# Kernel tuning notes

Measured on AMD Instinct MI355X. Metric: run time of the kernel, lower is better.

Reference implementation:

```python
import jax, jax.numpy as jnp
import numpy as np

EPS = 1e-06


def setup_inputs() -> dict:
    key = jax.random.key(0)
    B, T, M = 64, 8000, 80
    x = jax.random.uniform(key, (B, T, M), dtype=jnp.float32)
    # learned params are stored in log-space, per-mel, matching the torch module
    log_s = jnp.full((M,), np.log(0.0001), dtype=jnp.float32)
    log_alpha = jnp.full((M,), np.log(0.98), dtype=jnp.float32)
    log_delta = jnp.full((M,), np.log(2.0), dtype=jnp.float32)
    log_r = jnp.full((M,), np.log(0.2), dtype=jnp.float32)
    return {"x": x, "log_s": log_s, "log_alpha": log_alpha,
            "log_delta": log_delta, "log_r": log_r}


def reference(x, log_s, log_alpha, log_delta, log_r):
    # PCEN: leaky-integrator EMA over time + power-law compression.
    s = jnp.exp(log_s)          # [M]
    alpha = jnp.exp(log_alpha)  # [M]
    delta = jnp.exp(log_delta)  # [M]
    r = jnp.exp(log_r)          # [M]
    delta_r = delta ** r

    B, T, M = x.shape
    xt = jnp.swapaxes(x, 0, 1)  # [T, B, M] so scan streams over time

    def step(m_prev, frame):  # m_prev, frame: [B, M]
        m_cur = (1.0 - s) * m_prev + s * frame
        out = (frame / (m_cur + EPS) ** alpha + delta) ** r - delta_r
        return m_cur, out

    m0 = jnp.zeros((B, M), dtype=x.dtype)
    _, out_t = jax.lax.scan(step, m0, xt)  # [T, B, M]
    return jnp.swapaxes(out_t, 0, 1)       # [B, T, M]
```

## Files before the change

kernel.cpp:

```cpp
#include <hip/hip_runtime.h>
#include <math.h>

#define PCEN_EPS 1e-6f


__global__ void pcen_chunk_scan_v4(const float4* __restrict__ x,
                                   const float* __restrict__ log_s,
                                   float4* __restrict__ contrib,
                                   int B, int T, int M4, int C, int L) {
    int tid = blockIdx.x * blockDim.x + threadIdx.x;
    int total = B * C * M4;
    if (tid >= total) return;
    int g = tid % M4;
    int c = (tid / M4) % C;
    int b = tid / (M4 * C);

    float sx = expf(log_s[4 * g + 0]);
    float sy = expf(log_s[4 * g + 1]);
    float sz = expf(log_s[4 * g + 2]);
    float sw = expf(log_s[4 * g + 3]);
    float ox = 1.0f - sx, oy = 1.0f - sy, oz = 1.0f - sz, ow = 1.0f - sw;

    int start = c * L;
    int len = T - start;
    if (len > L) len = L;
    if (len < 0) len = 0;

    int base = (b * T + start) * M4 + g;
    float mx = 0.0f, my = 0.0f, mz = 0.0f, mw = 0.0f;
#pragma unroll 8
    for (int i = 0; i < len; ++i) {
        float4 xv = x[base];
        mx = fmaf(ox, mx, sx * xv.x);
        my = fmaf(oy, my, sy * xv.y);
        mz = fmaf(oz, mz, sz * xv.z);
        mw = fmaf(ow, mw, sw * xv.w);
        base += M4;
    }
    float4 o;
    o.x = mx; o.y = my; o.z = mz; o.w = mw;
    contrib[tid] = o;
}

__global__ void pcen_chunk_prefix_v4(const float4* __restrict__ contrib,
                                     const float* __restrict__ log_s,
                                     float4* __restrict__ m_start,
                                     int B, int T, int M4, int C, int L) {
    int tid = blockIdx.x * blockDim.x + threadIdx.x;
    if (tid >= B * M4) return;
    int g = tid % M4;
    int b = tid / M4;

    float sx = expf(log_s[4 * g + 0]);
    float sy = expf(log_s[4 * g + 1]);
    float sz = expf(log_s[4 * g + 2]);
    float sw = expf(log_s[4 * g + 3]);
    float ox = 1.0f - sx, oy = 1.0f - sy, oz = 1.0f - sz, ow = 1.0f - sw;
    float dxf = powf(ox, (float)L);
    float dyf = powf(oy, (float)L);
    float dzf = powf(oz, (float)L);
    float dwf = powf(ow, (float)L);

    int base = b * C * M4 + g;
    float mx = 0.0f, my = 0.0f, mz = 0.0f, mw = 0.0f;
#pragma unroll 4
    for (int c = 0; c < C; ++c) {
        float4 o;
        o.x = mx; o.y = my; o.z = mz; o.w = mw;
        m_start[base + c * M4] = o;

        int start = c * L;
        int len = T - start;
        if (len > L) len = L;
        if (len < 0) len = 0;

        float fx = dxf, fy = dyf, fz = dzf, fw = dwf;
        if (len != L) {
            fx = powf(ox, (float)len);
            fy = powf(oy, (float)len);
            fz = powf(oz, (float)len);
            fw = powf(ow, (float)len);
        }
        float4 cv = contrib[base + c * M4];
        mx = fmaf(fx, mx, cv.x);
        my = fmaf(fy, my, cv.y);
        mz = fmaf(fz, mz, cv.z);
        mw = fmaf(fw, mw, cv.w);
    }
}

__global__ void pcen_output_v4(const float4* __restrict__ x,
                               const float* __restrict__ log_s,
                               const float* __restrict__ log_alpha,
                               const float* __restrict__ log_delta,
                               const float* __restrict__ log_r,
                               const float4* __restrict__ m_start,
                               float4* __restrict__ out,
                               int B, int T, int M4, int C, int L) {
    int tid = blockIdx.x * blockDim.x + threadIdx.x;
    int total = B * C * M4;
    if (tid >= total) return;
    int g = tid % M4;
    int c = (tid / M4) % C;
    int b = tid / (M4 * C);

    float sx = expf(log_s[4 * g + 0]);
    float sy = expf(log_s[4 * g + 1]);
    float sz = expf(log_s[4 * g + 2]);
    float sw = expf(log_s[4 * g + 3]);
    float ox = 1.0f - sx, oy = 1.0f - sy, oz = 1.0f - sz, ow = 1.0f - sw;

    float ax = expf(log_alpha[4 * g + 0]);
    float ay = expf(log_alpha[4 * g + 1]);
    float az = expf(log_alpha[4 * g + 2]);
    float aw = expf(log_alpha[4 * g + 3]);

    float dx = expf(log_delta[4 * g + 0]);
    float dy = expf(log_delta[4 * g + 1]);
    float dz = expf(log_delta[4 * g + 2]);
    float dw = expf(log_delta[4 * g + 3]);

    float rx = expf(log_r[4 * g + 0]);
    float ry = expf(log_r[4 * g + 1]);
    float rz = expf(log_r[4 * g + 2]);
    float rw = expf(log_r[4 * g + 3]);

    float drx = powf(dx, rx);
    float dry = powf(dy, ry);
    float drz = powf(dz, rz);
    float drw = powf(dw, rw);

    int start = c * L;
    int len = T - start;
    if (len > L) len = L;
    if (len < 0) len = 0;

    float4 m0 = m_start[tid];
    float mx = m0.x, my = m0.y, mz = m0.z, mw = m0.w;

    int base = (b * T + start) * M4 + g;
#pragma unroll 4
    for (int i = 0; i < len; ++i) {
        float4 xv = x[base];
        mx = fmaf(ox, mx, sx * xv.x);
        my = fmaf(oy, my, sy * xv.y);
        mz = fmaf(oz, mz, sz * xv.z);
        mw = fmaf(ow, mw, sw * xv.w);

        float4 o;
        float px = __expf(-ax * __logf(mx + PCEN_EPS));
        float py = __expf(-ay * __logf(my + PCEN_EPS));
        float pz = __expf(-az * __logf(mz + PCEN_EPS));
        float pw = __expf(-aw * __logf(mw + PCEN_EPS));
        float yx = fmaf(xv.x, px, dx);
        float yy = fmaf(xv.y, py, dy);
        float yz = fmaf(xv.z, pz, dz);
        float yw = fmaf(xv.w, pw, dw);
        o.x = __expf(rx * __logf(yx)) - drx;
        o.y = __expf(ry * __logf(yy)) - dry;
        o.z = __expf(rz * __logf(yz)) - drz;
        o.w = __expf(rw * __logf(yw)) - drw;

        out[base] = o;
        base += M4;
    }
}


__global__ void pcen_chunk_scan(const float* __restrict__ x,
                                const float* __restrict__ log_s,
                                float* __restrict__ contrib,
                                int B, int T, int M, int C, int L) {
    int tid = blockIdx.x * blockDim.x + threadIdx.x;
    int total = B * C * M;
    if (tid >= total) return;
    int mi = tid % M;
    int c  = (tid / M) % C;
    int b  = tid / (M * C);

    float s   = expf(log_s[mi]);
    float oms = 1.0f - s;

    int start = c * L;
    int len = T - start;
    if (len > L) len = L;
    if (len < 0) len = 0;

    int base = (b * T + start) * M + mi;
    float m = 0.0f;
#pragma unroll 4
    for (int i = 0; i < len; ++i) {
        m = fmaf(oms, m, s * x[base]);
        base += M;
    }
    contrib[tid] = m;
}

__global__ void pcen_chunk_prefix(const float* __restrict__ contrib,
                                  const float* __restrict__ log_s,
                                  float* __restrict__ m_start,
                                  int B, int T, int M, int C, int L) {
    int tid = blockIdx.x * blockDim.x + threadIdx.x;
    if (tid >= B * M) return;
    int mi = tid % M;
    int b  = tid / M;

    float s   = expf(log_s[mi]);
    float oms = 1.0f - s;
    float dL_full = powf(oms, (float)L);

    int base = b * C * M + mi;
    float m = 0.0f;
    for (int c = 0; c < C; ++c) {
        m_start[base + c * M] = m;
        int start = c * L;
        int len = T - start;
        if (len > L) len = L;
        if (len < 0) len = 0;
        float dL = (len == L) ? dL_full : powf(oms, (float)len);
        m = fmaf(dL, m, contrib[base + c * M]);
    }
}

__global__ void pcen_output(const float* __restrict__ x,
                            const float* __restrict__ log_s,
                            const float* __restrict__ log_alpha,
                            const float* __restrict__ log_delta,
                            const float* __restrict__ log_r,
                            const float* __restrict__ m_start,
                            float* __restrict__ out,
                            int B, int T, int M, int C, int L) {
    int tid = blockIdx.x * blockDim.x + threadIdx.x;
    int total = B * C * M;
    if (tid >= total) return;
    int mi = tid % M;
    int c  = (tid / M) % C;
    int b  = tid / (M * C);

    float s     = expf(log_s[mi]);
    float alpha = expf(log_alpha[mi]);
    float delta = expf(log_delta[mi]);
    float r     = expf(log_r[mi]);
    float delta_r = powf(delta, r);
    float oms   = 1.0f - s;

    int start = c * L;
    int len = T - start;
    if (len > L) len = L;
    if (len < 0) len = 0;

    float m = m_start[tid];
    int base = (b * T + start) * M + mi;
#pragma unroll 4
    for (int i = 0; i < len; ++i) {
        float xv = x[base];
        m = fmaf(oms, m, s * xv);
        float p = __expf(-alpha * __logf(m + PCEN_EPS));
        float y = fmaf(xv, p, delta);
        out[base] = __expf(r * __logf(y)) - delta_r;
        base += M;
    }
}

extern "C" void kernel_launch(void* const* d_in, const int* in_sizes, int n_in,
                              void* d_out, int out_size, void* d_ws, size_t ws_size,
                              hipStream_t stream) {
    const float* x         = (const float*)d_in[0];
    const float* log_s     = (const float*)d_in[1];
    const float* log_alpha = (const float*)d_in[2];
    const float* log_delta = (const float*)d_in[3];
    const float* log_r     = (const float*)d_in[4];
    float* out = (float*)d_out;

    const int M = in_sizes[1];
    const int B = 64;
    const int T = in_sizes[0] / (B * M);

    int C = 200;
    while (C > 1 && (size_t)(2ll * B * C * M * 4) > ws_size) C--;
    const int L = (T + C - 1) / C;

    float* contrib = (float*)d_ws;
    float* mstart  = contrib + (size_t)B * C * M;

    const int threads = 256;

    if ((M & 3) == 0) {
        const int M4 = M / 4;
        int total1 = B * C * M4;
        int total2 = B * M4;
        pcen_chunk_scan_v4<<<(total1 + threads - 1) / threads, threads, 0, stream>>>(
            (const float4*)x, log_s, (float4*)contrib, B, T, M4, C, L);
        pcen_chunk_prefix_v4<<<(total2 + threads - 1) / threads, threads, 0, stream>>>(
            (const float4*)contrib, log_s, (float4*)mstart, B, T, M4, C, L);
        pcen_output_v4<<<(total1 + threads - 1) / threads, threads, 0, stream>>>(
            (const float4*)x, log_s, log_alpha, log_delta, log_r,
            (const float4*)mstart, (float4*)out, B, T, M4, C, L);
    } else {
        int total1 = B * C * M;
        int total2 = B * M;
        pcen_chunk_scan<<<(total1 + threads - 1) / threads, threads, 0, stream>>>(
            x, log_s, contrib, B, T, M, C, L);
        pcen_chunk_prefix<<<(total2 + threads - 1) / threads, threads, 0, stream>>>(
            contrib, log_s, mstart, B, T, M, C, L);
        pcen_output<<<(total1 + threads - 1) / threads, threads, 0, stream>>>(
            x, log_s, log_alpha, log_delta, log_r, mstart, out, B, T, M, C, L);
    }
}
```

Before: 393.6 us.

## Fuse chunked PCEN scan into single-pass decoupled look-back kernel

Replaces the three-kernel chunk scan, prefix and output pipeline with one kernel. Blocks take a dynamic ticket and publish per-chunk aggregates and inclusive prefixes with status flags, and later chunks resolve their starting state by look-back over earlier chunks. This removes a kernel launch and the global round-trip of the contrib and m_start buffers. It adds a reset kernel, spin-waiting on atomics, and serial look-back latency. The fallback path's chunk count also changes.

```diff
diff --git a/kernel.cpp b/kernel.cpp
--- a/kernel.cpp
+++ b/kernel.cpp
@@ -3,145 +3,118 @@
 
 #define PCEN_EPS 1e-6f
 
-
-__global__ void pcen_chunk_scan_v4(const float4* __restrict__ x,
-                                   const float* __restrict__ log_s,
-                                   float4* __restrict__ contrib,
-                                   int B, int T, int M4, int C, int L) {
-    int tid = blockIdx.x * blockDim.x + threadIdx.x;
-    int total = B * C * M4;
-    if (tid >= total) return;
-    int g = tid % M4;
-    int c = (tid / M4) % C;
-    int b = tid / (M4 * C);
-
-    float sx = expf(log_s[4 * g + 0]);
-    float sy = expf(log_s[4 * g + 1]);
-    float sz = expf(log_s[4 * g + 2]);
-    float sw = expf(log_s[4 * g + 3]);
-    float ox = 1.0f - sx, oy = 1.0f - sy, oz = 1.0f - sz, ow = 1.0f - sw;
-
-    int start = c * L;
+__global__ void pcen_reset(int* __restrict__ p, int n) {
+    int i = blockIdx.x * blockDim.x + threadIdx.x;
+    int stride = gridDim.x * blockDim.x;
+    for (; i < n; i += stride) p[i] = 0;
+}
+
+__global__ __launch_bounds__(256) void pcen_fused_v4(
+    const float4* __restrict__ x,
+    const float* __restrict__ log_s,
+    const float* __restrict__ log_alpha,
+    const float* __restrict__ log_delta,
+    const float* __restrict__ log_r,
+    float4* __restrict__ aggbuf,
+    float4* __restrict__ inclbuf,
+    int* __restrict__ status,
+    int* __restrict__ ticket,
+    float4* __restrict__ out,
+    int B, int T, int G, int C, int L)
+{
+    __shared__ int svb;
+    if (threadIdx.x == 0) svb = atomicAdd(ticket, 1);
+    __syncthreads();
+    const int vtid = svb * (int)blockDim.x + (int)threadIdx.x;
+    const int BG = B * G;
+    const int c = vtid / BG;
+    if (c >= C) return;
+    const int rem = vtid - c * BG;
+    const int b = rem / G;
+    const int g = rem - b * G;
+
+    const float4 lsv = ((const float4*)log_s)[g];
+    const float sx = expf(lsv.x), sy = expf(lsv.y), sz = expf(lsv.z), sw = expf(lsv.w);
+    const float ox = 1.0f - sx, oy = 1.0f - sy, oz = 1.0f - sz, ow = 1.0f - sw;
+
+    const int start = c * L;
     int len = T - start;
     if (len > L) len = L;
     if (len < 0) len = 0;
 
-    int base = (b * T + start) * M4 + g;
-    float mx = 0.0f, my = 0.0f, mz = 0.0f, mw = 0.0f;
+    const int base0 = (b * T + start) * G + g;
+    float mx = 0.f, my = 0.f, mz = 0.f, mw = 0.f;
+    {
+        int p = base0;
 #pragma unroll 8
-    for (int i = 0; i < len; ++i) {
-        float4 xv = x[base];
-        mx = fmaf(ox, mx, sx * xv.x);
-        my = fmaf(oy, my, sy * xv.y);
-        mz = fmaf(oz, mz, sz * xv.z);
-        mw = fmaf(ow, mw, sw * xv.w);
-        base += M4;
-    }
-    float4 o;
-    o.x = mx; o.y = my; o.z = mz; o.w = mw;
-    contrib[tid] = o;
-}
-
-__global__ void pcen_chunk_prefix_v4(const float4* __restrict__ contrib,
-                                     const float* __restrict__ log_s,
-                                     float4* __restrict__ m_start,
-                                     int B, int T, int M4, int C, int L) {
-    int tid = blockIdx.x * blockDim.x + threadIdx.x;
-    if (tid >= B * M4) return;
-    int g = tid % M4;
-    int b = tid / M4;
-
-    float sx = expf(log_s[4 * g + 0]);
-    float sy = expf(log_s[4 * g + 1]);
-    float sz = expf(log_s[4 * g + 2]);
-    float sw = expf(log_s[4 * g + 3]);
-    float ox = 1.0f - sx, oy = 1.0f - sy, oz = 1.0f - sz, ow = 1.0f - sw;
-    float dxf = powf(ox, (float)L);
-    float dyf = powf(oy, (float)L);
-    float dzf = powf(oz, (float)L);
-    float dwf = powf(ow, (float)L);
-
-    int base = b * C * M4 + g;
-    float mx = 0.0f, my = 0.0f, mz = 0.0f, mw = 0.0f;
-#pragma unroll 4
-    for (int c = 0; c < C; ++c) {
-        float4 o;
-        o.x = mx; o.y = my; o.z = mz; o.w = mw;
-        m_start[base + c * M4] = o;
-
-        int start = c * L;
-        int len = T - start;
-        if (len > L) len = L;
-        if (len < 0) len = 0;
-
-        float fx = dxf, fy = dyf, fz = dzf, fw = dwf;
-        if (len != L) {
-            fx = powf(ox, (float)len);
-            fy = powf(oy, (float)len);
-            fz = powf(oz, (float)len);
-            fw = powf(ow, (float)len);
-        }
-        float4 cv = contrib[base + c * M4];
-        mx = fmaf(fx, mx, cv.x);
-        my = fmaf(fy, my, cv.y);
-        mz = fmaf(fz, mz, cv.z);
-        mw = fmaf(fw, mw, cv.w);
-    }
-}
-
-__global__ void pcen_output_v4(const float4* __restrict__ x,
-                               const float* __restrict__ log_s,
-                               const float* __restrict__ log_alpha,
-                               const float* __restrict__ log_delta,
-                               const float* __restrict__ log_r,
-                               const float4* __restrict__ m_start,
-                               float4* __restrict__ out,
-                               int B, int T, int M4, int C, int L) {
-    int tid = blockIdx.x * blockDim.x + threadIdx.x;
-    int total = B * C * M4;
-    if (tid >= total) return;
-    int g = tid % M4;
-    int c = (tid / M4) % C;
-    int b = tid / (M4 * C);
-
-    float sx = expf(log_s[4 * g + 0]);
-    float sy = expf(log_s[4 * g + 1]);
-    float sz = expf(log_s[4 * g + 2]);
-    float sw = expf(log_s[4 * g + 3]);
-    float ox = 1.0f - sx, oy = 1.0f - sy, oz = 1.0f - sz, ow = 1.0f - sw;
-
-    float ax = expf(log_alpha[4 * g + 0]);
-    float ay = expf(log_alpha[4 * g + 1]);
-    float az = expf(log_alpha[4 * g + 2]);
-    float aw = expf(log_alpha[4 * g + 3]);
-
-    float dx = expf(log_delta[4 * g + 0]);
-    float dy = expf(log_delta[4 * g + 1]);
-    float dz = expf(log_delta[4 * g + 2]);
-    float dw = expf(log_delta[4 * g + 3]);
-
-    float rx = expf(log_r[4 * g + 0]);
-    float ry = expf(log_r[4 * g + 1]);
-    float rz = expf(log_r[4 * g + 2]);
-    float rw = expf(log_r[4 * g + 3]);
-
-    float drx = powf(dx, rx);
-    float dry = powf(dy, ry);
-    float drz = powf(dz, rz);
-    float drw = powf(dw, rw);
-
-    int start = c * L;
-    int len = T - start;
-    if (len > L) len = L;
-    if (len < 0) len = 0;
-
-    float4 m0 = m_start[tid];
-    float mx = m0.x, my = m0.y, mz = m0.z, mw = m0.w;
-
-    int base = (b * T + start) * M4 + g;
+        for (int i = 0; i < len; ++i) {
+            float4 xv = x[p];
+            mx = fmaf(ox, mx, sx * xv.x);
+            my = fmaf(oy, my, sy * xv.y);
+            mz = fmaf(oz, mz, sz * xv.z);
+            mw = fmaf(ow, mw, sw * xv.w);
+            p += G;
+        }
+    }
+    const int sidx = vtid;
+    float4 a; a.x = mx; a.y = my; a.z = mz; a.w = mw;
+    aggbuf[sidx] = a;
+    if (c == 0) {
+        inclbuf[sidx] = a;
+        __hip_atomic_store(&status[sidx], 2, __ATOMIC_RELEASE, __HIP_MEMORY_SCOPE_AGENT);
+    } else {
+        __hip_atomic_store(&status[sidx], 1, __ATOMIC_RELEASE, __HIP_MEMORY_SCOPE_AGENT);
+    }
+
+    const float dLx = powf(ox, (float)L);
+    const float dLy = powf(oy, (float)L);
+    const float dLz = powf(oz, (float)L);
+    const float dLw = powf(ow, (float)L);
+    float msx = 0.f, msy = 0.f, msz = 0.f, msw = 0.f;
+    if (c > 0) {
+        float wx = 1.f, wy = 1.f, wz = 1.f, ww = 1.f;
+        int j = c - 1;
+        while (j >= 0) {
+            const int jidx = j * BG + rem;
+            int st;
+            while ((st = __hip_atomic_load(&status[jidx], __ATOMIC_ACQUIRE,
+                                           __HIP_MEMORY_SCOPE_AGENT)) == 0) {
+                __builtin_amdgcn_s_sleep(1);
+            }
+            const float4 v = (st == 2) ? inclbuf[jidx] : aggbuf[jidx];
+            msx = fmaf(wx, v.x, msx);
+            msy = fmaf(wy, v.y, msy);
+            msz = fmaf(wz, v.z, msz);
+            msw = fmaf(ww, v.w, msw);
+            if (st == 2) break;
+            wx *= dLx; wy *= dLy; wz *= dLz; ww *= dLw;
+            --j;
+        }
+        if (c < C - 1) {
+            float4 ic;
+            ic.x = fmaf(dLx, msx, a.x);
+            ic.y = fmaf(dLy, msy, a.y);
+            ic.z = fmaf(dLz, msz, a.z);
+            ic.w = fmaf(dLw, msw, a.w);
+            inclbuf[sidx] = ic;
+            __hip_atomic_store(&status[sidx], 2, __ATOMIC_RELEASE, __HIP_MEMORY_SCOPE_AGENT);
+        }
+    }
+
+    const float4 lav = ((const float4*)log_alpha)[g];
+    const float4 ldv = ((const float4*)log_delta)[g];
+    const float4 lrv = ((const float4*)log_r)[g];
+    const float ax = expf(lav.x), ay = expf(lav.y), az = expf(lav.z), aw = expf(lav.w);
+    const float dx = expf(ldv.x), dy = expf(ldv.y), dz = expf(ldv.z), dw = expf(ldv.w);
+    const float rx = expf(lrv.x), ry = expf(lrv.y), rz = expf(lrv.z), rw = expf(lrv.w);
+    const float drx = powf(dx, rx), dry = powf(dy, ry);
+    const float drz = powf(dz, rz), drw = powf(dw, rw);
+
+    mx = msx; my = msy; mz = msz; mw = msw;
+    int p = base0;
 #pragma unroll 4
     for (int i = 0; i < len; ++i) {
-        float4 xv = x[base];
+        float4 xv = x[p];
         mx = fmaf(ox, mx, sx * xv.x);
         my = fmaf(oy, my, sy * xv.y);
         mz = fmaf(oz, mz, sz * xv.z);
@@ -161,11 +134,10 @@
         o.z = __expf(rz * __logf(yz)) - drz;
         o.w = __expf(rw * __logf(yw)) - drw;
 
-        out[base] = o;
-        base += M4;
-    }
-}
-
+        out[p] = o;
+        p += G;
+    }
+}
 
 __global__ void pcen_chunk_scan(const float* __restrict__ x,
                                 const float* __restrict__ log_s,
@@ -276,27 +248,43 @@
     const int B = 64;
     const int T = in_sizes[0] / (B * M);
 
-    int C = 200;
-    while (C > 1 && (size_t)(2ll * B * C * M * 4) > ws_size) C--;
-    const int L = (T + C - 1) / C;
-
-    float* contrib = (float*)d_ws;
-    float* mstart  = contrib + (size_t)B * C * M;
-
-    const int threads = 256;
-
     if ((M & 3) == 0) {
-        const int M4 = M / 4;
-        int total1 = B * C * M4;
-        int total2 = B * M4;
-        pcen_chunk_scan_v4<<<(total1 + threads - 1) / threads, threads, 0, stream>>>(
-            (const float4*)x, log_s, (float4*)contrib, B, T, M4, C, L);
-        pcen_chunk_prefix_v4<<<(total2 + threads - 1) / threads, threads, 0, stream>>>(
-            (const float4*)contrib, log_s, (float4*)mstart, B, T, M4, C, L);
-        pcen_output_v4<<<(total1 + threads - 1) / threads, threads, 0, stream>>>(
+        const int G = M / 4;
+        int C = 200;
+        while (C > 1) {
+            long long N = (long long)B * C * G;
+            if ((size_t)(N * 36ll + 256) <= ws_size) break;
+            --C;
+        }
+        int L = (T + C - 1) / C;
+        C = (T + L - 1) / L;
+        const long long N = (long long)B * C * G;
+
+        float4* aggbuf  = (float4*)d_ws;
+        float4* inclbuf = aggbuf + N;
+        int*    status  = (int*)(inclbuf + N);
+        int*    ticket  = status + N;
+
+        const int nz = (int)N + 16;
+        int zgrid = (nz + 256 * 4 - 1) / (256 * 4);
+        if (zgrid < 1) zgrid = 1;
+        pcen_reset<<<zgrid, 256, 0, stream>>>(status, nz);
+
+        const int total = (int)N;
+        const int blocks = (total + 255) / 256;
+        pcen_fused_v4<<<blocks, 256, 0, stream>>>(
             (const float4*)x, log_s, log_alpha, log_delta, log_r,
-            (const float4*)mstart, (float4*)out, B, T, M4, C, L);
+            aggbuf, inclbuf, status, ticket, (float4*)out,
+            B, T, G, C, L);
     } else {
+        int C = 50;
+        while (C > 1 && (size_t)(2ll * B * C * M * 4) > ws_size) C--;
+        const int L = (T + C - 1) / C;
+
+        float* contrib = (float*)d_ws;
+        float* mstart  = contrib + (size_t)B * C * M;
+
+        const int threads = 256;
         int total1 = B * C * M;
         int total2 = B * M;
         pcen_chunk_scan<<<(total1 + threads - 1) / threads, threads, 0, stream>>>(
```

Result: slower. 1.133 ms (+188.0%).
